# Optimization experiments

Hardware: AMD Instinct MI355X
Metric: run time of the kernel (lower is better)

## Reference

```python
import jax, jax.numpy as jnp
import numpy as np

N_EMBD = 1024
D_FF = 4 * N_EMBD
RANK = 4
NUM_LOOPS = 4
SCALE = 1.0 / RANK  # alpha=1.0 / r=4


def setup_inputs() -> dict:
    key = jax.random.key(0)
    ks = jax.random.split(key, 8)
    B, T = 8, 2048
    x = jax.random.normal(ks[0], (B, T, N_EMBD), dtype=jnp.float32)
    # base linears (torch nn.Linear weight layout: [out, in]), bias=False
    W1 = jax.random.normal(ks[1], (D_FF, N_EMBD), dtype=jnp.float32) * (1.0 / np.sqrt(N_EMBD))
    W2 = jax.random.normal(ks[2], (N_EMBD, D_FF), dtype=jnp.float32) * (1.0 / np.sqrt(D_FF))
    # LoRA factors: A [num_loops, r, in], B [num_loops, out, r]
    # (torch inits lora_B to zeros; we use small random values so the LoRA path is exercised)
    A1 = jax.random.normal(ks[3], (NUM_LOOPS, RANK, N_EMBD), dtype=jnp.float32) * (1.0 / np.sqrt(N_EMBD))
    B1 = jax.random.normal(ks[4], (NUM_LOOPS, D_FF, RANK), dtype=jnp.float32) * 0.01
    A2 = jax.random.normal(ks[5], (NUM_LOOPS, RANK, D_FF), dtype=jnp.float32) * (1.0 / np.sqrt(D_FF))
    B2 = jax.random.normal(ks[6], (NUM_LOOPS, N_EMBD, RANK), dtype=jnp.float32) * 0.01
    adapter_id = 1
    return {"x": x, "W1": W1, "A1": A1, "B1": B1, "W2": W2, "A2": A2, "B2": B2,
            "adapter_id": adapter_id}


def _lora_linear(x, W, A, B, adapter_id):
    # base: x @ W.T  (torch F.linear)
    out = jnp.einsum('btd,fd->btf', x, W)
    Aa = A[adapter_id]  # [r, in]
    Ba = B[adapter_id]  # [out, r]
    # low-rank correction: ((x @ A.T) @ B.T) * scale
    delta = jnp.einsum('btr,fr->btf', jnp.einsum('btd,rd->btr', x, Aa), Ba) * SCALE
    return out + delta


def reference(x, W1, A1, B1, W2, A2, B2, adapter_id):
    h = jax.nn.relu(_lora_linear(x, W1, A1, B1, adapter_id))
    out = _lora_linear(h, W2, A2, B2, adapter_id)
    # Dropout in eval mode (identity); see notes.
    return out
```

## Files before the change

kernel.cpp:

```cpp
#include <hip/hip_runtime.h>
#include <stdint.h>

typedef __bf16 bf16;
typedef __attribute__((ext_vector_type(8))) __bf16 bf16x8;
typedef __attribute__((ext_vector_type(4))) float f32x4;

#define LORA_SCALE 0.25f

__device__ __forceinline__ void gload_lds16(const bf16* g, bf16* l) {
    __builtin_amdgcn_global_load_lds(
        (const __attribute__((address_space(1))) uint32_t*)g,
        (__attribute__((address_space(3))) uint32_t*)l,
        16, 0, 0);
}

__device__ __forceinline__ bf16x8 cvt8(const float* p) {
    f32x4 a = *(const f32x4*)p;
    f32x4 b = *(const f32x4*)(p + 4);
    bf16x8 r;
    r[0] = (bf16)a[0]; r[1] = (bf16)a[1]; r[2] = (bf16)a[2]; r[3] = (bf16)a[3];
    r[4] = (bf16)b[0]; r[5] = (bf16)b[1]; r[6] = (bf16)b[2]; r[7] = (bf16)b[3];
    return r;
}

__global__ __launch_bounds__(256)
void cvt_weights(const float* __restrict__ in1, bf16* __restrict__ out1, int n1,
                 const float* __restrict__ in2, bf16* __restrict__ out2, int n2) {
    const int64_t idx = (int64_t)(blockIdx.x * 256 + threadIdx.x) * 8;
    if (idx < n1) *(bf16x8*)&out1[idx] = cvt8(&in1[idx]);
    else          *(bf16x8*)&out2[idx - n1] = cvt8(&in2[idx - n1]);
}

__global__ __launch_bounds__(256)
void lora1(const float* __restrict__ X, const float* __restrict__ Aall,
           const int* __restrict__ adapter, float* __restrict__ T,
           bf16* __restrict__ Xb)
{
    const int K = 1024;
    const int gid = blockIdx.x * 256 + threadIdx.x;
    const int aid = adapter[0];
    const float* Aa = Aall + (int64_t)aid * 4 * K;
    const int wid  = gid >> 6;
    const int lane = threadIdx.x & 63;
    const int m0   = wid * 4;

    float acc[4][4];
    #pragma unroll
    for (int rr = 0; rr < 4; rr++)
        #pragma unroll
        for (int r = 0; r < 4; r++) acc[rr][r] = 0.f;

    #pragma unroll
    for (int it = 0; it < K / 512; it++) {
        const int k = it * 512 + lane * 8;
        float av[4][8];
        #pragma unroll
        for (int r = 0; r < 4; r++) {
            f32x4 a = *(const f32x4*)&Aa[r * K + k];
            f32x4 b = *(const f32x4*)&Aa[r * K + k + 4];
            av[r][0]=a[0]; av[r][1]=a[1]; av[r][2]=a[2]; av[r][3]=a[3];
            av[r][4]=b[0]; av[r][5]=b[1]; av[r][6]=b[2]; av[r][7]=b[3];
        }
        #pragma unroll
        for (int rr = 0; rr < 4; rr++) {
            const float* xp = X + (int64_t)(m0 + rr) * K + k;
            f32x4 a = *(const f32x4*)xp;
            f32x4 b = *(const f32x4*)(xp + 4);
            float xv[8] = {a[0],a[1],a[2],a[3],b[0],b[1],b[2],b[3]};
            bf16x8 xb;
            #pragma unroll
            for (int e = 0; e < 8; e++) xb[e] = (bf16)xv[e];
            *(bf16x8*)&Xb[(int64_t)(m0 + rr) * K + k] = xb;
            #pragma unroll
            for (int r = 0; r < 4; r++)
                #pragma unroll
                for (int e = 0; e < 8; e++)
                    acc[rr][r] += xv[e] * av[r][e];
        }
    }
    #pragma unroll
    for (int rr = 0; rr < 4; rr++)
        #pragma unroll
        for (int r = 0; r < 4; r++)
            #pragma unroll
            for (int off = 32; off >= 1; off >>= 1)
                acc[rr][r] += __shfl_xor(acc[rr][r], off);
    if (lane == 0) {
        #pragma unroll
        for (int rr = 0; rr < 4; rr++) {
            f32x4 t;
            t[0] = acc[rr][0]; t[1] = acc[rr][1]; t[2] = acc[rr][2]; t[3] = acc[rr][3];
            *(f32x4*)&T[(int64_t)(m0 + rr) * 4] = t;
        }
    }
}

__global__ __launch_bounds__(256)
void t2_reduce(const float* __restrict__ T2p, float* __restrict__ T2,
               int M, int NP) {
    const int i = blockIdx.x * 256 + threadIdx.x;
    float s = 0.f;
    for (int p = 0; p < NP; p++) s += T2p[(int64_t)p * M * 4 + i];
    T2[i] = s;
}

#define MFMA16(AF, BF, JOFF)                                                     \
    __builtin_amdgcn_s_setprio(1);                                              \
    _Pragma("unroll")                                                            \
    for (int mi = 0; mi < 4; mi++)                                               \
        _Pragma("unroll")                                                        \
        for (int j = 0; j < 4; j++)                                              \
            acc[mi][JOFF + j] = __builtin_amdgcn_mfma_f32_16x16x32_bf16(         \
                AF[mi], BF[j], acc[mi][JOFF + j], 0, 0, 0);                      \
    __builtin_amdgcn_s_setprio(0);

template<bool RELU, typename CT, int PART, bool FUSET2>
__global__ __launch_bounds__(512, 2)
void gemm_lora9(const bf16* __restrict__ A,
                const bf16* __restrict__ Bm,
                CT* __restrict__ C,
                const float* __restrict__ Tlo,
                const float* __restrict__ Blo,
                const int* __restrict__ adapter,
                const float* __restrict__ A2,
                float* __restrict__ T2p,
                int M, int N, int K)
{
    __shared__ alignas(16) bf16 smem[65536];

    const int tid  = threadIdx.x;
    const int lane = tid & 63;
    const int w    = tid >> 6;
    const int quad = lane >> 4;
    const int l16  = lane & 15;

    int bx, by;
    {
        const int Nt = gridDim.x, Mt = gridDim.y;
        const int id = blockIdx.y * Nt + blockIdx.x;
        const int xcd = id & 7, k = id >> 3;
        if (PART == 0) { const int q = Nt >> 3; bx = xcd * q + (k % q); by = k / q; }
        else           { const int q = Mt >> 3; bx = k % Nt; by = xcd * q + (k / Nt); }
    }
    const int nBase = bx * 256;
    const int mBase = by * 256;
    const int wm = (w >> 1) * 64;
    const int wn = (w & 1) * 128;

    f32x4 acc[4][8];
    #pragma unroll
    for (int i = 0; i < 4; i++)
        #pragma unroll
        for (int j = 0; j < 8; j++)
            #pragma unroll
            for (int e = 0; e < 4; e++) acc[i][j][e] = 0.f;

    const bf16* gA = A  + (int64_t)mBase * K;
    const bf16* gB = Bm + (int64_t)nBase * K;

    const int sq    = (tid & 3) ^ ((tid >> 3) & 3);
    const int srow  = ((tid >> 3) << 1) | ((tid >> 2) & 1);
    const bf16* sA0 = gA + (int64_t)srow * K + sq * 8;
    const bf16* sA1 = gA + (int64_t)(srow + 128) * K + sq * 8;
    const bf16* sB0 = gB + (int64_t)srow * K + sq * 8;
    const bf16* sB1 = gB + (int64_t)(srow + 128) * K + sq * 8;
    const int dstW  = w * 512;

    const int pc8  = (quad ^ ((l16 >> 1) & 3)) * 8;
    const int aOff = (wm + l16) * 32 + pc8;
    const int bOff = (wn + l16) * 32 + pc8;

    const int NT = K >> 6;

    auto stage = [&](const bf16* s0, const bf16* s1, int t, int uidx) {
        bf16* u = smem + ((t & 1) * 4 + uidx) * 8192;
        const int co = t * 64 + (uidx >> 1) * 32;
        gload_lds16(s0 + co, u + dstW);
        gload_lds16(s1 + co, u + dstW + 4096);
    };

    stage(sA0, sA1, 0, 0); stage(sB0, sB1, 0, 1);
    stage(sA0, sA1, 0, 2); stage(sB0, sB1, 0, 3);
    if (NT > 1) {
        stage(sA0, sA1, 1, 0); stage(sB0, sB1, 1, 1); stage(sA0, sA1, 1, 2);
        asm volatile("s_waitcnt vmcnt(6)" ::: "memory");
    } else {
        asm volatile("s_waitcnt vmcnt(0)" ::: "memory");
    }
    __builtin_amdgcn_s_barrier();
    __builtin_amdgcn_sched_barrier(0);

    bf16x8 aX[4], aY[4], bX[4], bY[4];
    {
        const bf16* p0 = smem;
        const bf16* p1 = smem + 8192;
        #pragma unroll
        for (int i = 0; i < 4; i++) aX[i] = *(const bf16x8*)&p0[aOff + i * 512];
        #pragma unroll
        for (int j = 0; j < 4; j++) bX[j] = *(const bf16x8*)&p1[bOff + j * 512];
    }

    for (int t = 0; t < NT; ++t) {
        const bf16* ub = smem + (t & 1) * 32768;
        const bf16* u1 = ub + 8192;
        const bf16* u2 = ub + 16384;
        const bf16* u3 = ub + 24576;
        const bf16* n0 = smem + ((t + 1) & 1) * 32768;
        const bf16* n1 = n0 + 8192;
        const bool sNext  = (t + 1 < NT);
        const bool sNext2 = (t + 2 < NT);

        asm volatile("s_waitcnt lgkmcnt(0)" ::: "memory");
        __builtin_amdgcn_sched_barrier(0);
        #pragma unroll
        for (int j = 0; j < 4; j++) bY[j] = *(const bf16x8*)&u1[bOff + (4 + j) * 512];
        if (sNext) stage(sB0, sB1, t + 1, 3);
        MFMA16(aX, bX, 0)
        __builtin_amdgcn_s_barrier();
        __builtin_amdgcn_sched_barrier(0);

        asm volatile("s_waitcnt lgkmcnt(0)" ::: "memory");
        __builtin_amdgcn_sched_barrier(0);
        #pragma unroll
        for (int i = 0; i < 4; i++) aY[i] = *(const bf16x8*)&u2[aOff + i * 512];
        #pragma unroll
        for (int j = 0; j < 4; j++) bX[j] = *(const bf16x8*)&u3[bOff + j * 512];
        if (sNext2) stage(sA0, sA1, t + 2, 0);
        MFMA16(aX, bY, 4)
        __builtin_amdgcn_s_barrier();
        __builtin_amdgcn_sched_barrier(0);

        asm volatile("s_waitcnt lgkmcnt(0)" ::: "memory");
        __builtin_amdgcn_sched_barrier(0);
        #pragma unroll
        for (int j = 0; j < 4; j++) bY[j] = *(const bf16x8*)&u3[bOff + (4 + j) * 512];
        if (sNext2) stage(sB0, sB1, t + 2, 1);
        if (sNext2)      asm volatile("s_waitcnt vmcnt(4)" ::: "memory");
        else if (sNext)  asm volatile("s_waitcnt vmcnt(0)" ::: "memory");
        MFMA16(aY, bX, 0)
        __builtin_amdgcn_s_barrier();
        __builtin_amdgcn_sched_barrier(0);

        asm volatile("s_waitcnt lgkmcnt(0)" ::: "memory");
        __builtin_amdgcn_sched_barrier(0);
        if (sNext) {
            #pragma unroll
            for (int i = 0; i < 4; i++) aX[i] = *(const bf16x8*)&n0[aOff + i * 512];
            #pragma unroll
            for (int j = 0; j < 4; j++) bX[j] = *(const bf16x8*)&n1[bOff + j * 512];
        }
        if (sNext2) stage(sA0, sA1, t + 2, 2);
        MFMA16(aY, bY, 4)
        __builtin_amdgcn_s_barrier();
        __builtin_amdgcn_sched_barrier(0);
    }

    const int aid = adapter[0];
    const float* Ba = Blo + (int64_t)aid * N * 4;

    f32x4 bv[8];
    #pragma unroll
    for (int j = 0; j < 8; j++) {
        const int f = nBase + wn + j * 16 + l16;
        bv[j] = *(const f32x4*)&Ba[(int64_t)f * 4];
    }

    float a2v[8][4];
    if constexpr (FUSET2) {
        const float* A2a = A2 + (int64_t)aid * 4 * N;
        #pragma unroll
        for (int j = 0; j < 8; j++) {
            const int f = nBase + wn + j * 16 + l16;
            #pragma unroll
            for (int r2 = 0; r2 < 4; r2++)
                a2v[j][r2] = A2a[(int64_t)r2 * N + f];
        }
    }
    float* T2row = FUSET2 ? T2p + (int64_t)(bx * 2 + (w & 1)) * M * 4 : nullptr;

    if constexpr (sizeof(CT) == 2) {
        bf16* scratch = smem + w * (16 * 136);
        #pragma unroll
        for (int mi = 0; mi < 4; mi++) {
            f32x4 tv[4];
            #pragma unroll
            for (int r = 0; r < 4; r++) {
                const int m = mBase + wm + mi * 16 + quad * 4 + r;
                tv[r] = *(const f32x4*)&Tlo[(int64_t)m * 4];
            }
            float tp[4][4];
            if constexpr (FUSET2)
                #pragma unroll
                for (int r = 0; r < 4; r++)
                    #pragma unroll
                    for (int r2 = 0; r2 < 4; r2++) tp[r][r2] = 0.f;
            #pragma unroll
            for (int j = 0; j < 8; j++) {
                #pragma unroll
                for (int r = 0; r < 4; r++) {
                    const float d = tv[r][0] * bv[j][0] + tv[r][1] * bv[j][1]
                                  + tv[r][2] * bv[j][2] + tv[r][3] * bv[j][3];
                    float v = acc[mi][j][r] + LORA_SCALE * d;
                    if (RELU) v = v > 0.f ? v : 0.f;
                    if constexpr (FUSET2)
                        #pragma unroll
                        for (int r2 = 0; r2 < 4; r2++) tp[r][r2] += v * a2v[j][r2];
                    scratch[(quad * 4 + r) * 136 + j * 16 + l16] = (bf16)v;
                }
            }
            if constexpr (FUSET2) {
                #pragma unroll
                for (int r = 0; r < 4; r++)
                    #pragma unroll
                    for (int r2 = 0; r2 < 4; r2++)
                        #pragma unroll
                        for (int off = 8; off >= 1; off >>= 1)
                            tp[r][r2] += __shfl_xor(tp[r][r2], off);
                if (l16 == 0) {
                    #pragma unroll
                    for (int r = 0; r < 4; r++) {
                        const int m = mBase + wm + mi * 16 + quad * 4 + r;
                        f32x4 o;
                        o[0] = tp[r][0]; o[1] = tp[r][1];
                        o[2] = tp[r][2]; o[3] = tp[r][3];
                        *(f32x4*)&T2row[(int64_t)m * 4] = o;
                    }
                }
            }
            #pragma unroll
            for (int it = 0; it < 4; it++) {
                const int cid = it * 64 + lane;
                const int row = cid >> 4, c8 = cid & 15;
                bf16x8 vv = *(const bf16x8*)&scratch[row * 136 + c8 * 8];
                const int m = mBase + wm + mi * 16 + row;
                *(bf16x8*)&C[(int64_t)m * N + nBase + wn + c8 * 8] = vv;
            }
        }
    } else {
        float* scratchf = (float*)smem + w * (16 * 132);
        #pragma unroll
        for (int mi = 0; mi < 4; mi++) {
            f32x4 tv[4];
            #pragma unroll
            for (int r = 0; r < 4; r++) {
                const int m = mBase + wm + mi * 16 + quad * 4 + r;
                tv[r] = *(const f32x4*)&Tlo[(int64_t)m * 4];
            }
            #pragma unroll
            for (int j = 0; j < 8; j++) {
                #pragma unroll
                for (int r = 0; r < 4; r++) {
                    const float d = tv[r][0] * bv[j][0] + tv[r][1] * bv[j][1]
                                  + tv[r][2] * bv[j][2] + tv[r][3] * bv[j][3];
                    float v = acc[mi][j][r] + LORA_SCALE * d;
                    if (RELU) v = v > 0.f ? v : 0.f;
                    scratchf[(quad * 4 + r) * 132 + j * 16 + l16] = v;
                }
            }
            #pragma unroll
            for (int it = 0; it < 8; it++) {
                const int cid = it * 64 + lane;
                const int row = cid >> 5, c4 = cid & 31;
                f32x4 vv = *(const f32x4*)&scratchf[row * 132 + c4 * 4];
                const int m = mBase + wm + mi * 16 + row;
                *(f32x4*)&C[(int64_t)m * N + nBase + wn + c4 * 4] = vv;
            }
        }
    }
}

extern "C" void kernel_launch(void* const* d_in, const int* in_sizes, int n_in,
                              void* d_out, int out_size, void* d_ws, size_t ws_size,
                              hipStream_t stream) {
    const float* x  = (const float*)d_in[0];
    const float* W1 = (const float*)d_in[1];
    const float* A1 = (const float*)d_in[2];
    const float* B1 = (const float*)d_in[3];
    const float* W2 = (const float*)d_in[4];
    const float* A2 = (const float*)d_in[5];
    const float* B2 = (const float*)d_in[6];
    const int* adapter = (const int*)d_in[7];
    float* out = (float*)d_out;

    const int M = 16384, D = 1024, F = 4096;
    const int Nt1 = F / 256;

    bf16*  h   = (bf16*)d_ws;
    bf16*  xb  = h + (size_t)M * F;
    bf16*  wb1 = xb + (size_t)M * D;
    bf16*  wb2 = wb1 + (size_t)F * D;
    float* t1  = (float*)(wb2 + (size_t)D * F);
    float* t2  = t1 + (size_t)M * 4;
    float* t2p = t2 + (size_t)M * 4;

    lora1<<<M / 16, 256, 0, stream>>>(x, A1, adapter, t1, xb);
    cvt_weights<<<(2 * F * D) / 2048, 256, 0, stream>>>(W1, wb1, F * D, W2, wb2, D * F);
    dim3 g1(F / 256, M / 256);
    gemm_lora9<true, bf16, 0, true><<<g1, 512, 0, stream>>>(
        xb, wb1, h, t1, B1, adapter, A2, t2p, M, F, D);
    t2_reduce<<<(M * 4) / 256, 256, 0, stream>>>(t2p, t2, M, 2 * Nt1);
    dim3 g2(D / 256, M / 256);
    gemm_lora9<false, float, 1, false><<<g2, 512, 0, stream>>>(
        h, wb2, out, t2, B2, adapter, nullptr, nullptr, M, D, F);
}
```

Before: 430.7 us.

## Make first GEMM blocks loop over four N-tiles and prefetch across the tile boundary

The first GEMM kernel now runs a quarter as many blocks. Each block walks four consecutive 256-wide N tiles while keeping the same A row panel. The first pipeline stages for the next tile are issued during the current tile's epilogue, which now writes its bf16 scratch into the second LDS buffer to make room. This aims to cut block launch and prologue cost and improve A-panel reuse. The trade-off is only 256 blocks for 2 slots per CU, so co-resident blocks can no longer hide each other's epilogues.

```diff
diff --git a/kernel.cpp b/kernel.cpp
--- a/kernel.cpp
+++ b/kernel.cpp
@@ -114,17 +114,17 @@
                 AF[mi], BF[j], acc[mi][JOFF + j], 0, 0, 0);                      \
     __builtin_amdgcn_s_setprio(0);
 
-template<bool RELU, typename CT, int PART, bool FUSET2>
+template<bool RELU, typename CT, bool FUSET2, int NSUB>
 __global__ __launch_bounds__(512, 2)
-void gemm_lora9(const bf16* __restrict__ A,
-                const bf16* __restrict__ Bm,
-                CT* __restrict__ C,
-                const float* __restrict__ Tlo,
-                const float* __restrict__ Blo,
-                const int* __restrict__ adapter,
-                const float* __restrict__ A2,
-                float* __restrict__ T2p,
-                int M, int N, int K)
+void gemm_p(const bf16* __restrict__ A,
+            const bf16* __restrict__ Bm,
+            CT* __restrict__ C,
+            const float* __restrict__ Tlo,
+            const float* __restrict__ Blo,
+            const int* __restrict__ adapter,
+            const float* __restrict__ A2,
+            float* __restrict__ T2p,
+            int M, int N, int K)
 {
     __shared__ alignas(16) bf16 smem[65536];
 
@@ -136,35 +136,29 @@
 
     int bx, by;
     {
-        const int Nt = gridDim.x, Mt = gridDim.y;
-        const int id = blockIdx.y * Nt + blockIdx.x;
+        const int id = blockIdx.y * gridDim.x + blockIdx.x;
         const int xcd = id & 7, k = id >> 3;
-        if (PART == 0) { const int q = Nt >> 3; bx = xcd * q + (k % q); by = k / q; }
-        else           { const int q = Mt >> 3; bx = k % Nt; by = xcd * q + (k / Nt); }
+        const int nGrp = gridDim.x;
+        const int q = gridDim.y >> 3;
+        by = xcd * q + (k / nGrp);
+        bx = (k % nGrp) * NSUB;
     }
-    const int nBase = bx * 256;
     const int mBase = by * 256;
     const int wm = (w >> 1) * 64;
     const int wn = (w & 1) * 128;
 
     f32x4 acc[4][8];
-    #pragma unroll
-    for (int i = 0; i < 4; i++)
-        #pragma unroll
-        for (int j = 0; j < 8; j++)
-            #pragma unroll
-            for (int e = 0; e < 4; e++) acc[i][j][e] = 0.f;
-
-    const bf16* gA = A  + (int64_t)mBase * K;
-    const bf16* gB = Bm + (int64_t)nBase * K;
-
-    const int sq    = (tid & 3) ^ ((tid >> 3) & 3);
-    const int srow  = ((tid >> 3) << 1) | ((tid >> 2) & 1);
+
+    const bf16* gA = A + (int64_t)mBase * K;
+    const int sq   = (tid & 3) ^ ((tid >> 3) & 3);
+    const int srow = ((tid >> 3) << 1) | ((tid >> 2) & 1);
     const bf16* sA0 = gA + (int64_t)srow * K + sq * 8;
     const bf16* sA1 = gA + (int64_t)(srow + 128) * K + sq * 8;
+    const int dstW = w * 512;
+
+    const bf16* gB = Bm + (int64_t)bx * 256 * K;
     const bf16* sB0 = gB + (int64_t)srow * K + sq * 8;
     const bf16* sB1 = gB + (int64_t)(srow + 128) * K + sq * 8;
-    const int dstW  = w * 512;
 
     const int pc8  = (quad ^ ((l16 >> 1) & 3)) * 8;
     const int aOff = (wm + l16) * 32 + pc8;
@@ -172,199 +166,226 @@
 
     const int NT = K >> 6;
 
-    auto stage = [&](const bf16* s0, const bf16* s1, int t, int uidx) {
-        bf16* u = smem + ((t & 1) * 4 + uidx) * 8192;
-        const int co = t * 64 + (uidx >> 1) * 32;
+    auto stageU = [&](const bf16* s0, const bf16* s1, int buf, int uidx, int co) {
+        bf16* u = smem + (buf * 4 + uidx) * 8192;
         gload_lds16(s0 + co, u + dstW);
         gload_lds16(s1 + co, u + dstW + 4096);
     };
 
-    stage(sA0, sA1, 0, 0); stage(sB0, sB1, 0, 1);
-    stage(sA0, sA1, 0, 2); stage(sB0, sB1, 0, 3);
-    if (NT > 1) {
-        stage(sA0, sA1, 1, 0); stage(sB0, sB1, 1, 1); stage(sA0, sA1, 1, 2);
-        asm volatile("s_waitcnt vmcnt(6)" ::: "memory");
-    } else {
-        asm volatile("s_waitcnt vmcnt(0)" ::: "memory");
-    }
+    stageU(sA0, sA1, 0, 0, 0);  stageU(sB0, sB1, 0, 1, 0);
+    stageU(sA0, sA1, 0, 2, 32); stageU(sB0, sB1, 0, 3, 32);
+    stageU(sA0, sA1, 1, 0, 64); stageU(sB0, sB1, 1, 1, 64);
+    stageU(sA0, sA1, 1, 2, 96);
+    asm volatile("s_waitcnt vmcnt(6)" ::: "memory");
     __builtin_amdgcn_s_barrier();
     __builtin_amdgcn_sched_barrier(0);
 
     bf16x8 aX[4], aY[4], bX[4], bY[4];
-    {
-        const bf16* p0 = smem;
-        const bf16* p1 = smem + 8192;
-        #pragma unroll
-        for (int i = 0; i < 4; i++) aX[i] = *(const bf16x8*)&p0[aOff + i * 512];
-        #pragma unroll
-        for (int j = 0; j < 4; j++) bX[j] = *(const bf16x8*)&p1[bOff + j * 512];
-    }
-
-    for (int t = 0; t < NT; ++t) {
-        const bf16* ub = smem + (t & 1) * 32768;
-        const bf16* u1 = ub + 8192;
-        const bf16* u2 = ub + 16384;
-        const bf16* u3 = ub + 24576;
-        const bf16* n0 = smem + ((t + 1) & 1) * 32768;
-        const bf16* n1 = n0 + 8192;
-        const bool sNext  = (t + 1 < NT);
-        const bool sNext2 = (t + 2 < NT);
-
-        asm volatile("s_waitcnt lgkmcnt(0)" ::: "memory");
-        __builtin_amdgcn_sched_barrier(0);
-        #pragma unroll
-        for (int j = 0; j < 4; j++) bY[j] = *(const bf16x8*)&u1[bOff + (4 + j) * 512];
-        if (sNext) stage(sB0, sB1, t + 1, 3);
-        MFMA16(aX, bX, 0)
-        __builtin_amdgcn_s_barrier();
-        __builtin_amdgcn_sched_barrier(0);
-
-        asm volatile("s_waitcnt lgkmcnt(0)" ::: "memory");
-        __builtin_amdgcn_sched_barrier(0);
-        #pragma unroll
-        for (int i = 0; i < 4; i++) aY[i] = *(const bf16x8*)&u2[aOff + i * 512];
-        #pragma unroll
-        for (int j = 0; j < 4; j++) bX[j] = *(const bf16x8*)&u3[bOff + j * 512];
-        if (sNext2) stage(sA0, sA1, t + 2, 0);
-        MFMA16(aX, bY, 4)
-        __builtin_amdgcn_s_barrier();
-        __builtin_amdgcn_sched_barrier(0);
-
-        asm volatile("s_waitcnt lgkmcnt(0)" ::: "memory");
-        __builtin_amdgcn_sched_barrier(0);
-        #pragma unroll
-        for (int j = 0; j < 4; j++) bY[j] = *(const bf16x8*)&u3[bOff + (4 + j) * 512];
-        if (sNext2) stage(sB0, sB1, t + 2, 1);
-        if (sNext2)      asm volatile("s_waitcnt vmcnt(4)" ::: "memory");
-        else if (sNext)  asm volatile("s_waitcnt vmcnt(0)" ::: "memory");
-        MFMA16(aY, bX, 0)
-        __builtin_amdgcn_s_barrier();
-        __builtin_amdgcn_sched_barrier(0);
-
-        asm volatile("s_waitcnt lgkmcnt(0)" ::: "memory");
-        __builtin_amdgcn_sched_barrier(0);
-        if (sNext) {
-            #pragma unroll
-            for (int i = 0; i < 4; i++) aX[i] = *(const bf16x8*)&n0[aOff + i * 512];
-            #pragma unroll
-            for (int j = 0; j < 4; j++) bX[j] = *(const bf16x8*)&n1[bOff + j * 512];
-        }
-        if (sNext2) stage(sA0, sA1, t + 2, 2);
-        MFMA16(aY, bY, 4)
-        __builtin_amdgcn_s_barrier();
-        __builtin_amdgcn_sched_barrier(0);
-    }
+    #pragma unroll
+    for (int i = 0; i < 4; i++) aX[i] = *(const bf16x8*)&smem[aOff + i * 512];
+    #pragma unroll
+    for (int j = 0; j < 4; j++) bX[j] = *(const bf16x8*)&smem[8192 + bOff + j * 512];
 
     const int aid = adapter[0];
-    const float* Ba = Blo + (int64_t)aid * N * 4;
-
-    f32x4 bv[8];
-    #pragma unroll
-    for (int j = 0; j < 8; j++) {
-        const int f = nBase + wn + j * 16 + l16;
-        bv[j] = *(const f32x4*)&Ba[(int64_t)f * 4];
-    }
-
-    float a2v[8][4];
-    if constexpr (FUSET2) {
-        const float* A2a = A2 + (int64_t)aid * 4 * N;
+    const float* Ba  = Blo + (int64_t)aid * N * 4;
+    const float* A2a = FUSET2 ? A2 + (int64_t)aid * 4 * N : nullptr;
+
+    #pragma unroll 1
+    for (int sub = 0; sub < NSUB; ++sub) {
+        #pragma unroll
+        for (int i = 0; i < 4; i++)
+            #pragma unroll
+            for (int j = 0; j < 8; j++)
+                #pragma unroll
+                for (int e = 0; e < 4; e++) acc[i][j][e] = 0.f;
+
+        for (int t = 0; t < NT; ++t) {
+            const bf16* ub = smem + (t & 1) * 32768;
+            const bf16* u1 = ub + 8192;
+            const bf16* u2 = ub + 16384;
+            const bf16* u3 = ub + 24576;
+            const bf16* n0 = smem + ((t + 1) & 1) * 32768;
+            const bf16* n1 = n0 + 8192;
+            const bool sNext  = (t + 1 < NT);
+            const bool sNext2 = (t + 2 < NT);
+
+            asm volatile("s_waitcnt lgkmcnt(0)" ::: "memory");
+            __builtin_amdgcn_sched_barrier(0);
+            #pragma unroll
+            for (int j = 0; j < 4; j++) bY[j] = *(const bf16x8*)&u1[bOff + (4 + j) * 512];
+            if (sNext) stageU(sB0, sB1, (t + 1) & 1, 3, (t + 1) * 64 + 32);
+            MFMA16(aX, bX, 0)
+            __builtin_amdgcn_s_barrier();
+            __builtin_amdgcn_sched_barrier(0);
+
+            asm volatile("s_waitcnt lgkmcnt(0)" ::: "memory");
+            __builtin_amdgcn_sched_barrier(0);
+            #pragma unroll
+            for (int i = 0; i < 4; i++) aY[i] = *(const bf16x8*)&u2[aOff + i * 512];
+            #pragma unroll
+            for (int j = 0; j < 4; j++) bX[j] = *(const bf16x8*)&u3[bOff + j * 512];
+            if (sNext2) stageU(sA0, sA1, t & 1, 0, (t + 2) * 64);
+            MFMA16(aX, bY, 4)
+            __builtin_amdgcn_s_barrier();
+            __builtin_amdgcn_sched_barrier(0);
+
+            asm volatile("s_waitcnt lgkmcnt(0)" ::: "memory");
+            __builtin_amdgcn_sched_barrier(0);
+            #pragma unroll
+            for (int j = 0; j < 4; j++) bY[j] = *(const bf16x8*)&u3[bOff + (4 + j) * 512];
+            if (sNext2) stageU(sB0, sB1, t & 1, 1, (t + 2) * 64);
+            if (sNext2)      asm volatile("s_waitcnt vmcnt(4)" ::: "memory");
+            else if (sNext)  asm volatile("s_waitcnt vmcnt(0)" ::: "memory");
+            MFMA16(aY, bX, 0)
+            __builtin_amdgcn_s_barrier();
+            __builtin_amdgcn_sched_barrier(0);
+
+            asm volatile("s_waitcnt lgkmcnt(0)" ::: "memory");
+            __builtin_amdgcn_sched_barrier(0);
+            if (t + 1 < NT) {
+                #pragma unroll
+                for (int i = 0; i < 4; i++) aX[i] = *(const bf16x8*)&n0[aOff + i * 512];
+                #pragma unroll
+                for (int j = 0; j < 4; j++) bX[j] = *(const bf16x8*)&n1[bOff + j * 512];
+            }
+            if (sNext2) stageU(sA0, sA1, t & 1, 2, (t + 2) * 64 + 32);
+            MFMA16(aY, bY, 4)
+            __builtin_amdgcn_s_barrier();
+            __builtin_amdgcn_sched_barrier(0);
+        }
+
+        const int nBase = bx * 256;
+
+        const bf16 *nB0 = nullptr, *nB1 = nullptr;
+        if (sub + 1 < NSUB) {
+            const bf16* gBn = Bm + (int64_t)(bx + 1) * 256 * K;
+            nB0 = gBn + (int64_t)srow * K + sq * 8;
+            nB1 = gBn + (int64_t)(srow + 128) * K + sq * 8;
+            stageU(sA0, sA1, 0, 0, 0);  stageU(nB0, nB1, 0, 1, 0);
+            stageU(sA0, sA1, 0, 2, 32); stageU(nB0, nB1, 0, 3, 32);
+        }
+
+        f32x4 bv[8];
         #pragma unroll
         for (int j = 0; j < 8; j++) {
             const int f = nBase + wn + j * 16 + l16;
-            #pragma unroll
-            for (int r2 = 0; r2 < 4; r2++)
-                a2v[j][r2] = A2a[(int64_t)r2 * N + f];
-        }
-    }
-    float* T2row = FUSET2 ? T2p + (int64_t)(bx * 2 + (w & 1)) * M * 4 : nullptr;
-
-    if constexpr (sizeof(CT) == 2) {
-        bf16* scratch = smem + w * (16 * 136);
-        #pragma unroll
-        for (int mi = 0; mi < 4; mi++) {
-            f32x4 tv[4];
-            #pragma unroll
-            for (int r = 0; r < 4; r++) {
-                const int m = mBase + wm + mi * 16 + quad * 4 + r;
-                tv[r] = *(const f32x4*)&Tlo[(int64_t)m * 4];
+            bv[j] = *(const f32x4*)&Ba[(int64_t)f * 4];
+        }
+        float a2v[8][4];
+        if constexpr (FUSET2) {
+            #pragma unroll
+            for (int j = 0; j < 8; j++) {
+                const int f = nBase + wn + j * 16 + l16;
+                #pragma unroll
+                for (int r2 = 0; r2 < 4; r2++)
+                    a2v[j][r2] = A2a[(int64_t)r2 * N + f];
             }
-            float tp[4][4];
-            if constexpr (FUSET2)
-                #pragma unroll
-                for (int r = 0; r < 4; r++)
+        }
+        float* T2row = FUSET2 ? T2p + (int64_t)(bx * 2 + (w & 1)) * M * 4 : nullptr;
+
+        if constexpr (sizeof(CT) == 2) {
+            bf16* scratch = smem + 32768 + w * (16 * 136);
+            #pragma unroll
+            for (int mi = 0; mi < 4; mi++) {
+                f32x4 tv[4];
+                #pragma unroll
+                for (int r = 0; r < 4; r++) {
+                    const int m = mBase + wm + mi * 16 + quad * 4 + r;
+                    tv[r] = *(const f32x4*)&Tlo[(int64_t)m * 4];
+                }
+                float tp[4][4];
+                if constexpr (FUSET2)
                     #pragma unroll
-                    for (int r2 = 0; r2 < 4; r2++) tp[r][r2] = 0.f;
-            #pragma unroll
-            for (int j = 0; j < 8; j++) {
-                #pragma unroll
-                for (int r = 0; r < 4; r++) {
-                    const float d = tv[r][0] * bv[j][0] + tv[r][1] * bv[j][1]
-                                  + tv[r][2] * bv[j][2] + tv[r][3] * bv[j][3];
-                    float v = acc[mi][j][r] + LORA_SCALE * d;
-                    if (RELU) v = v > 0.f ? v : 0.f;
-                    if constexpr (FUSET2)
+                    for (int r = 0; r < 4; r++)
                         #pragma unroll
-                        for (int r2 = 0; r2 < 4; r2++) tp[r][r2] += v * a2v[j][r2];
-                    scratch[(quad * 4 + r) * 136 + j * 16 + l16] = (bf16)v;
-                }
-            }
-            if constexpr (FUSET2) {
-                #pragma unroll
-                for (int r = 0; r < 4; r++)
-                    #pragma unroll
-                    for (int r2 = 0; r2 < 4; r2++)
-                        #pragma unroll
-                        for (int off = 8; off >= 1; off >>= 1)
-                            tp[r][r2] += __shfl_xor(tp[r][r2], off);
-                if (l16 == 0) {
+                        for (int r2 = 0; r2 < 4; r2++) tp[r][r2] = 0.f;
+                #pragma unroll
+                for (int j = 0; j < 8; j++) {
                     #pragma unroll
                     for (int r = 0; r < 4; r++) {
-                        const int m = mBase + wm + mi * 16 + quad * 4 + r;
-                        f32x4 o;
-                        o[0] = tp[r][0]; o[1] = tp[r][1];
-                        o[2] = tp[r][2]; o[3] = tp[r][3];
-                        *(f32x4*)&T2row[(int64_t)m * 4] = o;
+                        const float d = tv[r][0] * bv[j][0] + tv[r][1] * bv[j][1]
+                                      + tv[r][2] * bv[j][2] + tv[r][3] * bv[j][3];
+                        float v = acc[mi][j][r] + LORA_SCALE * d;
+                        if (RELU) v = v > 0.f ? v : 0.f;
+                        if constexpr (FUSET2)
+                            #pragma unroll
+                            for (int r2 = 0; r2 < 4; r2++) tp[r][r2] += v * a2v[j][r2];
+                        scratch[(quad * 4 + r) * 136 + j * 16 + l16] = (bf16)v;
                     }
                 }
+                if constexpr (FUSET2) {
+                    #pragma unroll
+                    for (int r = 0; r < 4; r++)
+                        #pragma unroll
+                        for (int r2 = 0; r2 < 4; r2++)
+                            #pragma unroll
+                            for (int off = 8; off >= 1; off >>= 1)
+                                tp[r][r2] += __shfl_xor(tp[r][r2], off);
+                    if (l16 == 0) {
+                        #pragma unroll
+                        for (int r = 0; r < 4; r++) {
+                            const int m = mBase + wm + mi * 16 + quad * 4 + r;
+                            f32x4 o;
+                            o[0] = tp[r][0]; o[1] = tp[r][1];
+                            o[2] = tp[r][2]; o[3] = tp[r][3];
+                            *(f32x4*)&T2row[(int64_t)m * 4] = o;
+                        }
+                    }
+                }
+                #pragma unroll
+                for (int it = 0; it < 4; it++) {
+                    const int cid = it * 64 + lane;
+                    const int row = cid >> 4, c8 = cid & 15;
+                    bf16x8 vv = *(const bf16x8*)&scratch[row * 136 + c8 * 8];
+                    const int m = mBase + wm + mi * 16 + row;
+                    *(bf16x8*)&C[(int64_t)m * N + nBase + wn + c8 * 8] = vv;
+                }
             }
-            #pragma unroll
-            for (int it = 0; it < 4; it++) {
-                const int cid = it * 64 + lane;
-                const int row = cid >> 4, c8 = cid & 15;
-                bf16x8 vv = *(const bf16x8*)&scratch[row * 136 + c8 * 8];
-                const int m = mBase + wm + mi * 16 + row;
-                *(bf16x8*)&C[(int64_t)m * N + nBase + wn + c8 * 8] = vv;
+        } else {
+            float* scratchf = (float*)smem + w * (16 * 132);
+            #pragma unroll
+            for (int mi = 0; mi < 4; mi++) {
+                f32x4 tv[4];
+                #pragma unroll
+                for (int r = 0; r < 4; r++) {
+                    const int m = mBase + wm + mi * 16 + quad * 4 + r;
+                    tv[r] = *(const f32x4*)&Tlo[(int64_t)m * 4];
+                }
+                #pragma unroll
+                for (int j = 0; j < 8; j++) {
+                    #pragma unroll
+                    for (int r = 0; r < 4; r++) {
+                        const float d = tv[r][0] * bv[j][0] + tv[r][1] * bv[j][1]
+                                      + tv[r][2] * bv[j][2] + tv[r][3] * bv[j][3];
+                        float v = acc[mi][j][r] + LORA_SCALE * d;
+                        if (RELU) v = v > 0.f ? v : 0.f;
+                        scratchf[(quad * 4 + r) * 132 + j * 16 + l16] = v;
+                    }
+                }
+                #pragma unroll
+                for (int it = 0; it < 8; it++) {
+                    const int cid = it * 64 + lane;
+                    const int row = cid >> 5, c4 = cid & 31;
+                    f32x4 vv = *(const f32x4*)&scratchf[row * 132 + c4 * 4];
+                    const int m = mBase + wm + mi * 16 + row;
+                    *(f32x4*)&C[(int64_t)m * N + nBase + wn + c4 * 4] = vv;
+                }
             }
         }
-    } else {
-        float* scratchf = (float*)smem + w * (16 * 132);
-        #pragma unroll
-        for (int mi = 0; mi < 4; mi++) {
-            f32x4 tv[4];
-            #pragma unroll
-            for (int r = 0; r < 4; r++) {
-                const int m = mBase + wm + mi * 16 + quad * 4 + r;
-                tv[r] = *(const f32x4*)&Tlo[(int64_t)m * 4];
-            }
-            #pragma unroll
-            for (int j = 0; j < 8; j++) {
-                #pragma unroll
-                for (int r = 0; r < 4; r++) {
-                    const float d = tv[r][0] * bv[j][0] + tv[r][1] * bv[j][1]
-                                  + tv[r][2] * bv[j][2] + tv[r][3] * bv[j][3];
-                    float v = acc[mi][j][r] + LORA_SCALE * d;
-                    if (RELU) v = v > 0.f ? v : 0.f;
-                    scratchf[(quad * 4 + r) * 132 + j * 16 + l16] = v;
-                }
-            }
-            #pragma unroll
-            for (int it = 0; it < 8; it++) {
-                const int cid = it * 64 + lane;
-                const int row = cid >> 5, c4 = cid & 31;
-                f32x4 vv = *(const f32x4*)&scratchf[row * 132 + c4 * 4];
-                const int m = mBase + wm + mi * 16 + row;
-                *(f32x4*)&C[(int64_t)m * N + nBase + wn + c4 * 4] = vv;
-            }
+
+        __syncthreads();
+
+        if (sub + 1 < NSUB) {
+            stageU(sA0, sA1, 1, 0, 64); stageU(nB0, nB1, 1, 1, 64);
+            stageU(sA0, sA1, 1, 2, 96);
+            asm volatile("s_waitcnt vmcnt(6)" ::: "memory");
+            __builtin_amdgcn_s_barrier();
+            __builtin_amdgcn_sched_barrier(0);
+            #pragma unroll
+            for (int i = 0; i < 4; i++) aX[i] = *(const bf16x8*)&smem[aOff + i * 512];
+            #pragma unroll
+            for (int j = 0; j < 4; j++) bX[j] = *(const bf16x8*)&smem[8192 + bOff + j * 512];
+            sB0 = nB0; sB1 = nB1; bx = bx + 1;
         }
     }
 }
@@ -395,11 +416,9 @@
 
     lora1<<<M / 16, 256, 0, stream>>>(x, A1, adapter, t1, xb);
     cvt_weights<<<(2 * F * D) / 2048, 256, 0, stream>>>(W1, wb1, F * D, W2, wb2, D * F);
-    dim3 g1(F / 256, M / 256);
-    gemm_lora9<true, bf16, 0, true><<<g1, 512, 0, stream>>>(
+    gemm_p<true, bf16, true, 4><<<dim3(F / 1024, M / 256), 512, 0, stream>>>(
         xb, wb1, h, t1, B1, adapter, A2, t2p, M, F, D);
     t2_reduce<<<(M * 4) / 256, 256, 0, stream>>>(t2p, t2, M, 2 * Nt1);
-    dim3 g2(D / 256, M / 256);
-    gemm_lora9<false, float, 1, false><<<g2, 512, 0, stream>>>(
+    gemm_p<false, float, false, 1><<<dim3(D / 256, M / 256), 512, 0, stream>>>(
         h, wb2, out, t2, B2, adapter, nullptr, nullptr, M, D, F);
 }
```

After: 542.0 us. 25.8% more time.
